# Kernel optimization log

Measured on AMD Instinct MI355X. Metric: run time of the kernel, lower is better.

Reference implementation:

```python
import jax, jax.numpy as jnp
import numpy as np
from jax import lax

H = 512          # hidden_dim
U = H // 2       # GRU units per direction
L = 3            # num_layers
B = 64           # num sequences
T = 512          # timesteps per sequence
EXTRA = 1000     # pass-through tail rows in `states`
RATE = 0.1       # dropout_rate
WSCALE = 0.05


def setup_inputs() -> dict:
    key = jax.random.key(0)
    ks = jax.random.split(key, 9)
    N = B * T + EXTRA
    states = jax.random.normal(ks[0], (N, H), jnp.float32)
    # prefix-valid mask: each sequence has a random valid length in [1, T]
    lengths = jax.random.randint(ks[1], (B,), 1, T + 1)
    mask2d = jnp.arange(T)[None, :] < lengths[:, None]          # [B, T]
    mask = jnp.concatenate([mask2d.reshape(-1), jnp.zeros((EXTRA,), bool)])
    # per-layer, per-direction GRU params (Keras reset_after=True layout):
    # kernel [H, 3U] (z|r|h), recurrent [U, 3U], bias [2, 3U] (input bias, recurrent bias)
    Wf = jax.random.normal(ks[2], (L, H, 3 * U), jnp.float32) * WSCALE
    Uf = jax.random.normal(ks[3], (L, U, 3 * U), jnp.float32) * WSCALE
    bf = jnp.zeros((L, 2, 3 * U), jnp.float32)
    Wb = jax.random.normal(ks[4], (L, H, 3 * U), jnp.float32) * WSCALE
    Ub = jax.random.normal(ks[5], (L, U, 3 * U), jnp.float32) * WSCALE
    bb = jnp.zeros((L, 2, 3 * U), jnp.float32)
    return {
        "states": states, "mask": mask, "seq_shape": (B, T), "training": 1,
        "Wf": Wf, "Uf": Uf, "bf": bf, "Wb": Wb, "Ub": Ub, "bb": bb,
    }


def _gru_scan(x, m, W, Uw, b):
    """Keras GRU (reset_after=True) over time with Keras mask semantics.
    x: [T, B, H], m: [T, B] bool. Returns outputs [T, B, U].
    Masked steps carry state (output = previous output)."""
    bi, br = b[0], b[1]
    xp = jnp.einsum('tbh,hk->tbk', x, W) + bi   # [T, B, 3U], hoisted input proj
    h0 = jnp.zeros((x.shape[1], U), x.dtype)

    def step(h, inp):
        xp_t, m_t = inp
        hp = h @ Uw + br                         # [B, 3U]
        xz, xr, xh = jnp.split(xp_t, 3, axis=-1)
        hz, hr, hh = jnp.split(hp, 3, axis=-1)
        z = jax.nn.sigmoid(xz + hz)
        r = jax.nn.sigmoid(xr + hr)
        hcand = jnp.tanh(xh + r * hh)
        hn = z * h + (1.0 - z) * hcand
        hn = jnp.where(m_t[:, None], hn, h)      # carry state through masked steps
        return hn, hn

    _, ys = lax.scan(step, h0, (xp, m))
    return ys


def _forward(states, mask, seq_shape, training, Wf, Uf, bf, Wb, Ub, bb):
    Bn, Tn = int(seq_shape[0]), int(seq_shape[1])
    total = Bn * Tn
    x = states[:total].reshape(Bn, Tn, H).transpose(1, 0, 2)  # [T, B, H]
    m = mask[:total].reshape(Bn, Tn).T                        # [T, B]
    rate = RATE * float(bool(training))
    dkey = jax.random.key(1234)
    for l in range(L):
        yf = _gru_scan(x, m, Wf[l], Uf[l], bf[l])
        yb = jnp.flip(_gru_scan(jnp.flip(x, 0), jnp.flip(m, 0), Wb[l], Ub[l], bb[l]), 0)
        x = jnp.concatenate([yf, yb], axis=-1)                # [T, B, H]
        if rate > 0.0:
            dkey, sk = jax.random.split(dkey)
            keep = jax.random.bernoulli(sk, 1.0 - rate, x.shape)
            x = jnp.where(keep, x / (1.0 - rate), 0.0)
    out = x.transpose(1, 0, 2).reshape(-1, H)                 # [B*T, H]
    return jnp.concatenate([out, states[total:]], axis=0)


def reference(states, mask, seq_shape, training, Wf, Uf, bf, Wb, Ub, bb):
    return _forward(states, mask, seq_shape, training, Wf, Uf, bf, Wb, Ub, bb)
```

## Files before the change

kernel.cpp:

```cpp
#include <hip/hip_runtime.h>
#include <stdint.h>

typedef __attribute__((ext_vector_type(8))) short short8;
typedef __attribute__((ext_vector_type(4))) float f32x4;

#define XB16_OFF  0UL
#define XP_OFF    33554432UL
#define WT_OFF    134217728UL
#define UT_OFF    138936320UL
#define BIASC_OFF 141295616UL
#define BRC_OFF   141314048UL
#define MASKT_OFF 141332480UL
#define FLAG_OFF  141725760UL

#define HB_STRIDE 264
#define HBLK (16 * HB_STRIDE)
#define LDS_BYTES (((size_t)256 * HB_STRIDE + 2 * HBLK) * 2)

#define LDS_BARRIER() asm volatile("s_waitcnt lgkmcnt(0)\n\ts_barrier" ::: "memory")

__host__ __device__ static inline void tf2x32(unsigned k0, unsigned k1,
                                              unsigned x0, unsigned x1,
                                              unsigned* o0, unsigned* o1) {
  unsigned ks2 = k0 ^ k1 ^ 0x1BD11BDAu;
#define TFR(r) { x0 += x1; x1 = (x1 << (r)) | (x1 >> (32 - (r))); x1 ^= x0; }
  x0 += k0; x1 += k1;
  TFR(13) TFR(15) TFR(26) TFR(6)   x0 += k1;  x1 += ks2 + 1u;
  TFR(17) TFR(29) TFR(16) TFR(24)  x0 += ks2; x1 += k0 + 2u;
  TFR(13) TFR(15) TFR(26) TFR(6)   x0 += k0;  x1 += k1 + 3u;
  TFR(17) TFR(29) TFR(16) TFR(24)  x0 += k1;  x1 += ks2 + 4u;
  TFR(13) TFR(15) TFR(26) TFR(6)   x0 += ks2; x1 += k0 + 5u;
#undef TFR
  *o0 = x0; *o1 = x1;
}

__device__ static inline short f2bf(float f) {
  unsigned u = __float_as_uint(f);
  u = (u + 0x7fffu + ((u >> 16) & 1u)) >> 16;
  return (short)u;
}
__device__ static inline float bf2f(short s) {
  unsigned u = ((unsigned)(unsigned short)s) << 16;
  return __uint_as_float(u);
}
__device__ static inline float cvt_lo(unsigned d) {
  union { unsigned short u; _Float16 h; } c; c.u = (unsigned short)(d & 0xffffu);
  return (float)c.h;
}
__device__ static inline float cvt_hi(unsigned d) {
  union { unsigned short u; _Float16 h; } c; c.u = (unsigned short)(d >> 16);
  return (float)c.h;
}

__global__ void init_k(unsigned* flag) {
  if (threadIdx.x == 0) *flag = 0u;
}

__global__ __launch_bounds__(256) void prep_k(
    const float* __restrict__ states, const unsigned* __restrict__ maskw,
    const float* __restrict__ Wf, const float* __restrict__ Uf,
    const float* __restrict__ bf_, const float* __restrict__ Wb,
    const float* __restrict__ Ub, const float* __restrict__ bb_,
    short* __restrict__ xb16, float* __restrict__ dout,
    short* __restrict__ Wt, short* __restrict__ Ut,
    float* __restrict__ biasc, float* __restrict__ brc,
    unsigned* __restrict__ flag) {
  const unsigned gid = blockIdx.x * 256 + threadIdx.x;
  {
    unsigned c = gid & 511u, rw = gid >> 9;
    unsigned t = rw >> 6, b = rw & 63u;
    xb16[gid] = f2bf(states[(size_t)(b * 512 + t) * 512 + c]);
  }
  if (gid < 512000u) dout[16777216u + gid] = states[16777216u + gid];
  if (gid < 2359296u) {
    unsigned l = gid / 786432u, rem = gid % 786432u;
    unsigned n = rem >> 9, k = rem & 511u;
    float s = (n < 768u) ? Wf[(size_t)(l * 512 + k) * 768 + n]
                         : Wb[(size_t)(l * 512 + k) * 768 + (n - 768u)];
    Wt[gid] = f2bf(s);
  }
  if (gid < 1179648u) {
    unsigned g = gid / 196608u, rem = gid % 196608u;
    unsigned dirv = g / 3u, l = g % 3u;
    unsigned n = rem >> 8, k = rem & 255u;
    const float* Usrc = dirv ? Ub : Uf;
    Ut[gid] = f2bf(Usrc[(size_t)(l * 256 + k) * 768 + n]);
  }
  if (gid < 4608u) {
    unsigned l = gid / 1536u, n = gid % 1536u;
    unsigned dirv = n / 768u, rem = n % 768u;
    const float* bsrc = dirv ? bb_ : bf_;
    float v = bsrc[(l * 2 + 0) * 768 + rem];
    if (rem < 512u) v += bsrc[(l * 2 + 1) * 768 + rem];
    biasc[gid] = v;
  }
  if (gid < 4608u) {
    unsigned g = gid / 768u, n = gid % 768u;
    unsigned dirv = g / 3u, l = g % 3u;
    brc[gid] = (dirv ? bb_ : bf_)[(l * 2 + 1) * 768 + n];
  }
  if (gid < 8192u) {
    if (maskw[gid] > 1u) atomicOr(flag, 1u);
  }
}

__global__ __launch_bounds__(256) void maskt_k(
    const unsigned char* __restrict__ mask8, const unsigned* __restrict__ flagp,
    unsigned char* __restrict__ maskt) {
  const unsigned gid = blockIdx.x * 256 + threadIdx.x;
  const unsigned b = gid >> 9, t = gid & 511u;
  const bool mbyte = (*flagp) != 0u;
  unsigned v = mbyte ? (unsigned)mask8[gid] : ((const unsigned*)mask8)[gid];
  maskt[t * 64 + b] = v ? 1u : 0u;
}

__global__ __launch_bounds__(256) void proj_gemm(
    const short* __restrict__ A, const short* __restrict__ Bt,
    const float* __restrict__ bias, _Float16* __restrict__ C) {
  __shared__ __align__(16) short As[4096];
  __shared__ __align__(16) short Bs[4096];
  const int tid = threadIdx.x;
  const int wave = tid >> 6, lane = tid & 63;
  const int col = lane & 15, kq = lane >> 4;
  const int wr = wave >> 1, wc = wave & 1;
  const int m0 = blockIdx.x * 128, n0 = blockIdx.y * 128;
  const uint4* Aq = (const uint4*)A;
  const uint4* Bq = (const uint4*)Bt;
  uint4* AsQ = (uint4*)As;
  uint4* BsQ = (uint4*)Bs;
  f32x4 acc[4][4];
#pragma unroll
  for (int i = 0; i < 4; ++i)
#pragma unroll
    for (int j = 0; j < 4; ++j) acc[i][j] = (f32x4){0.f, 0.f, 0.f, 0.f};

  for (int kt = 0; kt < 16; ++kt) {
    const int k8 = kt * 4;
#pragma unroll
    for (int rnd = 0; rnd < 2; ++rnd) {
      int chunk = rnd * 256 + tid;
      int row = chunk >> 2, kc = chunk & 3;
      AsQ[chunk] = Aq[(size_t)(m0 + row) * 64 + k8 + kc];
      BsQ[chunk] = Bq[(size_t)(n0 + row) * 64 + k8 + kc];
    }
    __syncthreads();
    short8 af[4], bfv[4];
#pragma unroll
    for (int i = 0; i < 4; ++i)
      af[i] = *(const short8*)(As + (wr * 64 + i * 16 + col) * 32 + kq * 8);
#pragma unroll
    for (int j = 0; j < 4; ++j)
      bfv[j] = *(const short8*)(Bs + (wc * 64 + j * 16 + col) * 32 + kq * 8);
#pragma unroll
    for (int i = 0; i < 4; ++i)
#pragma unroll
      for (int j = 0; j < 4; ++j)
        acc[i][j] = __builtin_amdgcn_mfma_f32_16x16x32_bf16(af[i], bfv[j], acc[i][j], 0, 0, 0);
    __syncthreads();
  }
#pragma unroll
  for (int j = 0; j < 4; ++j) {
    const int cg = n0 + wc * 64 + j * 16 + col;
    const float bv = bias[cg];
    const int dirv = cg / 768, rem = cg % 768;
    const int gate = rem >> 8, u = rem & 255;
    const size_t cbase =
        ((size_t)(((m0 >> 6) + wr) * 2 + dirv)) * 49152 + gate * 256 + u;
#pragma unroll
    for (int i = 0; i < 4; ++i) {
#pragma unroll
      for (int r = 0; r < 4; ++r)
        C[cbase + (size_t)(i * 16 + kq * 4 + r) * 768] = (_Float16)(acc[i][j][r] + bv);
    }
  }
}

__global__ __launch_bounds__(1024, 4) void gru16(
    const _Float16* __restrict__ xp, const short* __restrict__ UtAll,
    const float* __restrict__ brcAll, const unsigned char* __restrict__ maskt,
    short* __restrict__ yout, int layer) {
  extern __shared__ short lds[];
  short* hgate = lds;
  short* hbuf  = lds + 256 * HB_STRIDE;

  const int bid = blockIdx.x;
  const int dir = bid >> 2;
  const int b0 = (bid & 3) * 16;
  const int tid = threadIdx.x;
  const int wave = tid >> 6, lane = tid & 63;
  const int col = lane & 15, quad = lane >> 4;
  const int u0 = wave * 16 + quad * 4;
  const short* Ut = UtAll + (size_t)(dir * 3 + layer) * 768 * 256;
  const float* brc = brcAll + (dir * 3 + layer) * 768;

  const short* Uth = Ut + 512 * 256;
  for (int c = tid; c < 8192; c += 1024) {
    int row = c >> 5, q = c & 31;
    *(uint4*)(hgate + row * HB_STRIDE + q * 8) = *(const uint4*)(Uth + row * 256 + q * 8);
  }
  for (int i = tid; i < 2 * HBLK; i += 1024) hbuf[i] = 0;

  short8 zA[8], rA[8];
#pragma unroll
  for (int ks = 0; ks < 8; ++ks) {
    zA[ks] = *(const short8*)(Ut + (size_t)(wave * 16 + col) * 256 + ks * 32 + quad * 8);
    rA[ks] = *(const short8*)(Ut + (size_t)(256 + wave * 16 + col) * 256 + ks * 32 + quad * 8);
  }
  f32x4 brh;
#pragma unroll
  for (int r = 0; r < 4; ++r) brh[r] = brc[512 + u0 + r];

  const int t0 = dir ? 511 : 0;
  const int tstep = dir ? -1 : 1;
  const char* xpb = (const char*)xp;
  const int gb = b0 + col;
  unsigned xaddr = (unsigned)(((t0 * 2 + dir) * 64 + gb) * 1536 + wave * 32 + quad * 8);
  const int xstep = tstep * 196608;

  const short* hgA = hgate + (wave * 16 + col) * HB_STRIDE + quad * 8;
  const int rd_lane = col * HB_STRIDE + quad * 8;
  const int wr_lane = col * HB_STRIDE + u0;

  unsigned yoff = (unsigned)((t0 * 64 + gb) * 1024 + dir * 512 + u0 * 2);
  const int ystep = tstep * 65536;
  int moff = t0 * 64 + gb;

  uint2 pz, pr, ph;
  unsigned pm;
  pz = *(const uint2*)(xpb + xaddr);
  pr = *(const uint2*)(xpb + xaddr + 512);
  ph = *(const uint2*)(xpb + xaddr + 1024);
  pm = maskt[moff];

  float hp[4] = {0.f, 0.f, 0.f, 0.f};
  __syncthreads();

  for (int s = 0; s < 512; ++s) {
    f32x4 az, ar, ah;
    az[0] = cvt_lo(pz.x); az[1] = cvt_hi(pz.x);
    az[2] = cvt_lo(pz.y); az[3] = cvt_hi(pz.y);
    ar[0] = cvt_lo(pr.x); ar[1] = cvt_hi(pr.x);
    ar[2] = cvt_lo(pr.y); ar[3] = cvt_hi(pr.y);
    ah = brh;
    float xh[4];
    xh[0] = cvt_lo(ph.x); xh[1] = cvt_hi(ph.x);
    xh[2] = cvt_lo(ph.y); xh[3] = cvt_hi(ph.y);
    const bool mv = (pm != 0u);
    if (s < 511) {
      xaddr += xstep;
      pz = *(const uint2*)(xpb + xaddr);
      pr = *(const uint2*)(xpb + xaddr + 512);
      ph = *(const uint2*)(xpb + xaddr + 1024);
      moff += tstep * 64;
      pm = maskt[moff];
    }

    const short* hrd = hbuf + (s & 1) * HBLK + rd_lane;
#pragma unroll
    for (int ks = 0; ks < 8; ++ks) {
      short8 hbv = *(const short8*)(hrd + ks * 32);
      short8 hg  = *(const short8*)(hgA + ks * 32);
      az = __builtin_amdgcn_mfma_f32_16x16x32_bf16(zA[ks], hbv, az, 0, 0, 0);
      ar = __builtin_amdgcn_mfma_f32_16x16x32_bf16(rA[ks], hbv, ar, 0, 0, 0);
      ah = __builtin_amdgcn_mfma_f32_16x16x32_bf16(hg,     hbv, ah, 0, 0, 0);
    }

    float hn[4];
#pragma unroll
    for (int r = 0; r < 4; ++r) {
      float z  = 1.f / (1.f + __builtin_amdgcn_exp2f(az[r] * -1.44269504f));
      float rr = 1.f / (1.f + __builtin_amdgcn_exp2f(ar[r] * -1.44269504f));
      float pre = xh[r] + rr * ah[r];
      float hc = 1.f - 2.f / (__builtin_amdgcn_exp2f(pre * 2.88539008f) + 1.f);
      float hpv = hp[r];
      float v = hc + z * (hpv - hc);
      hn[r] = mv ? v : hpv;
      hp[r] = hn[r];
    }
    uint2 packed;
    asm("v_cvt_pk_bf16_f32 %0, %1, %2" : "=v"(packed.x) : "v"(hn[0]), "v"(hn[1]));
    asm("v_cvt_pk_bf16_f32 %0, %1, %2" : "=v"(packed.y) : "v"(hn[2]), "v"(hn[3]));
    *(uint2*)(hbuf + ((s & 1) ^ 1) * HBLK + wr_lane) = packed;
    *(uint2*)((char*)yout + yoff) = packed;
    yoff += ystep;
    LDS_BARRIER();
  }
}

__global__ __launch_bounds__(256) void drop_k(
    short* __restrict__ xb16, float* __restrict__ dout,
    const int* __restrict__ training, unsigned k0, unsigned k1, int last) {
  const unsigned gid = blockIdx.x * 256 + threadIdx.x;
  float v = bf2f(xb16[gid]);
  unsigned y0, y1;
  tf2x32(k0, k1, 0u, gid, &y0, &y1);
  unsigned bits = y0 ^ y1;
  float u = __uint_as_float((bits >> 9) | 0x3f800000u) - 1.0f;
  bool keep = u < 0.9f;
  int tr = *training;
  float ov = tr ? (keep ? v * (1.0f / 0.9f) : 0.0f) : v;
  if (last) {
    unsigned r = gid >> 9, c = gid & 511u;
    unsigned t = r >> 6, b = r & 63u;
    dout[(size_t)(b * 512 + t) * 512 + c] = ov;
  } else {
    xb16[gid] = f2bf(ov);
  }
}

extern "C" void kernel_launch(void* const* d_in, const int* in_sizes, int n_in,
                              void* d_out, int out_size, void* d_ws, size_t ws_size,
                              hipStream_t stream) {
  (void)in_sizes; (void)n_in; (void)out_size; (void)ws_size;
  const float* states = (const float*)d_in[0];
  const void*  mask   = d_in[1];
  const int*   training = (const int*)d_in[3];
  const float* Wf = (const float*)d_in[4];
  const float* Uf = (const float*)d_in[5];
  const float* bf_ = (const float*)d_in[6];
  const float* Wb = (const float*)d_in[7];
  const float* Ub = (const float*)d_in[8];
  const float* bb_ = (const float*)d_in[9];
  char* ws = (char*)d_ws;

  short* xb16   = (short*)(ws + XB16_OFF);
  _Float16* xp  = (_Float16*)(ws + XP_OFF);
  short* Wt     = (short*)(ws + WT_OFF);
  short* Ut     = (short*)(ws + UT_OFF);
  float* biasc  = (float*)(ws + BIASC_OFF);
  float* brc    = (float*)(ws + BRC_OFF);
  unsigned char* maskt = (unsigned char*)(ws + MASKT_OFF);
  unsigned* flag = (unsigned*)(ws + FLAG_OFF);
  float* dout = (float*)d_out;

  hipFuncSetAttribute((const void*)gru16,
                      hipFuncAttributeMaxDynamicSharedMemorySize, (int)LDS_BYTES);

  unsigned d0 = 0u, d1 = 1234u, sk0[3], sk1[3];
  for (int l = 0; l < 3; ++l) {
    unsigned a, b, c, d;
    tf2x32(d0, d1, 0u, 0u, &a, &b);
    tf2x32(d0, d1, 0u, 1u, &c, &d);
    sk0[l] = c; sk1[l] = d;
    d0 = a; d1 = b;
  }

  init_k<<<1, 64, 0, stream>>>(flag);
  prep_k<<<65536, 256, 0, stream>>>(states, (const unsigned*)mask, Wf, Uf, bf_,
                                    Wb, Ub, bb_, xb16, dout, Wt, Ut, biasc, brc, flag);
  maskt_k<<<128, 256, 0, stream>>>((const unsigned char*)mask, flag, maskt);
  for (int l = 0; l < 3; ++l) {
    proj_gemm<<<dim3(256, 12), 256, 0, stream>>>(xb16, Wt + (size_t)l * 1536 * 512,
                                                 biasc + l * 1536, xp);
    gru16<<<8, 1024, LDS_BYTES, stream>>>(xp, Ut, brc, maskt, xb16, l);
    drop_k<<<65536, 256, 0, stream>>>(xb16, dout, training, sk0[l], sk1[l], l == 2);
  }
}
```

Measured before the change: 3.797 ms.

## Halve GRU recurrence block to 8 waves, each computing 32 units

```diff
diff --git a/kernel.cpp b/kernel.cpp
--- a/kernel.cpp
+++ b/kernel.cpp
@@ -15,7 +15,7 @@
 
 #define HB_STRIDE 264
 #define HBLK (16 * HB_STRIDE)
-#define LDS_BYTES (((size_t)256 * HB_STRIDE + 2 * HBLK) * 2)
+#define LDS_BYTES (((size_t)128 * HB_STRIDE + 2 * HBLK) * 2)
 
 #define LDS_BARRIER() asm volatile("s_waitcnt lgkmcnt(0)\n\ts_barrier" ::: "memory")
 
@@ -175,13 +175,13 @@
   }
 }
 
-__global__ __launch_bounds__(1024, 4) void gru16(
+__global__ __launch_bounds__(512, 2) void gru32(
     const _Float16* __restrict__ xp, const short* __restrict__ UtAll,
     const float* __restrict__ brcAll, const unsigned char* __restrict__ maskt,
     short* __restrict__ yout, int layer) {
   extern __shared__ short lds[];
   short* hgate = lds;
-  short* hbuf  = lds + 256 * HB_STRIDE;
+  short* hbuf  = lds + 128 * HB_STRIDE;
 
   const int bid = blockIdx.x;
   const int dir = bid >> 2;
@@ -189,35 +189,44 @@
   const int tid = threadIdx.x;
   const int wave = tid >> 6, lane = tid & 63;
   const int col = lane & 15, quad = lane >> 4;
-  const int u0 = wave * 16 + quad * 4;
   const short* Ut = UtAll + (size_t)(dir * 3 + layer) * 768 * 256;
   const float* brc = brcAll + (dir * 3 + layer) * 768;
 
   const short* Uth = Ut + 512 * 256;
-  for (int c = tid; c < 8192; c += 1024) {
+  for (int c = tid; c < 4096; c += 512) {
     int row = c >> 5, q = c & 31;
-    *(uint4*)(hgate + row * HB_STRIDE + q * 8) = *(const uint4*)(Uth + row * 256 + q * 8);
-  }
-  for (int i = tid; i < 2 * HBLK; i += 1024) hbuf[i] = 0;
-
-  short8 zA[8], rA[8];
+    int u = ((row >> 4) << 5) + 16 + (row & 15);
+    *(uint4*)(hgate + row * HB_STRIDE + q * 8) = *(const uint4*)(Uth + u * 256 + q * 8);
+  }
+  for (int i = tid; i < 2 * HBLK; i += 512) hbuf[i] = 0;
+
+  short8 zA1[8], zA2[8], rA1[8], rA2[8], hA1[8];
+  const int m1 = wave * 32 + col;
 #pragma unroll
   for (int ks = 0; ks < 8; ++ks) {
-    zA[ks] = *(const short8*)(Ut + (size_t)(wave * 16 + col) * 256 + ks * 32 + quad * 8);
-    rA[ks] = *(const short8*)(Ut + (size_t)(256 + wave * 16 + col) * 256 + ks * 32 + quad * 8);
-  }
-  f32x4 brh;
-#pragma unroll
-  for (int r = 0; r < 4; ++r) brh[r] = brc[512 + u0 + r];
+    const int ko = ks * 32 + quad * 8;
+    zA1[ks] = *(const short8*)(Ut + (size_t)m1 * 256 + ko);
+    zA2[ks] = *(const short8*)(Ut + (size_t)(m1 + 16) * 256 + ko);
+    rA1[ks] = *(const short8*)(Ut + (size_t)(256 + m1) * 256 + ko);
+    rA2[ks] = *(const short8*)(Ut + (size_t)(256 + m1 + 16) * 256 + ko);
+    hA1[ks] = *(const short8*)(Ut + (size_t)(512 + m1) * 256 + ko);
+  }
+  const int u0 = wave * 32 + quad * 4;
+  f32x4 brh1, brh2;
+#pragma unroll
+  for (int r = 0; r < 4; ++r) {
+    brh1[r] = brc[512 + u0 + r];
+    brh2[r] = brc[512 + u0 + 16 + r];
+  }
 
   const int t0 = dir ? 511 : 0;
   const int tstep = dir ? -1 : 1;
   const char* xpb = (const char*)xp;
   const int gb = b0 + col;
-  unsigned xaddr = (unsigned)(((t0 * 2 + dir) * 64 + gb) * 1536 + wave * 32 + quad * 8);
+  unsigned xaddr = (unsigned)(((t0 * 2 + dir) * 64 + gb) * 1536 + wave * 64 + quad * 8);
   const int xstep = tstep * 196608;
 
-  const short* hgA = hgate + (wave * 16 + col) * HB_STRIDE + quad * 8;
+  const short* hg2 = hgate + (wave * 16 + col) * HB_STRIDE + quad * 8;
   const int rd_lane = col * HB_STRIDE + quad * 8;
   const int wr_lane = col * HB_STRIDE + u0;
 
@@ -225,32 +234,44 @@
   const int ystep = tstep * 65536;
   int moff = t0 * 64 + gb;
 
-  uint2 pz, pr, ph;
+  uint2 pz1, pz2, pr1, pr2, ph1, ph2;
   unsigned pm;
-  pz = *(const uint2*)(xpb + xaddr);
-  pr = *(const uint2*)(xpb + xaddr + 512);
-  ph = *(const uint2*)(xpb + xaddr + 1024);
+  pz1 = *(const uint2*)(xpb + xaddr);
+  pz2 = *(const uint2*)(xpb + xaddr + 32);
+  pr1 = *(const uint2*)(xpb + xaddr + 512);
+  pr2 = *(const uint2*)(xpb + xaddr + 544);
+  ph1 = *(const uint2*)(xpb + xaddr + 1024);
+  ph2 = *(const uint2*)(xpb + xaddr + 1056);
   pm = maskt[moff];
 
-  float hp[4] = {0.f, 0.f, 0.f, 0.f};
+  float hp[8] = {0.f, 0.f, 0.f, 0.f, 0.f, 0.f, 0.f, 0.f};
   __syncthreads();
 
   for (int s = 0; s < 512; ++s) {
-    f32x4 az, ar, ah;
-    az[0] = cvt_lo(pz.x); az[1] = cvt_hi(pz.x);
-    az[2] = cvt_lo(pz.y); az[3] = cvt_hi(pz.y);
-    ar[0] = cvt_lo(pr.x); ar[1] = cvt_hi(pr.x);
-    ar[2] = cvt_lo(pr.y); ar[3] = cvt_hi(pr.y);
-    ah = brh;
-    float xh[4];
-    xh[0] = cvt_lo(ph.x); xh[1] = cvt_hi(ph.x);
-    xh[2] = cvt_lo(ph.y); xh[3] = cvt_hi(ph.y);
+    f32x4 az1, az2, ar1, ar2, ah1, ah2;
+    az1[0] = cvt_lo(pz1.x); az1[1] = cvt_hi(pz1.x);
+    az1[2] = cvt_lo(pz1.y); az1[3] = cvt_hi(pz1.y);
+    az2[0] = cvt_lo(pz2.x); az2[1] = cvt_hi(pz2.x);
+    az2[2] = cvt_lo(pz2.y); az2[3] = cvt_hi(pz2.y);
+    ar1[0] = cvt_lo(pr1.x); ar1[1] = cvt_hi(pr1.x);
+    ar1[2] = cvt_lo(pr1.y); ar1[3] = cvt_hi(pr1.y);
+    ar2[0] = cvt_lo(pr2.x); ar2[1] = cvt_hi(pr2.x);
+    ar2[2] = cvt_lo(pr2.y); ar2[3] = cvt_hi(pr2.y);
+    ah1 = brh1; ah2 = brh2;
+    float xh[8];
+    xh[0] = cvt_lo(ph1.x); xh[1] = cvt_hi(ph1.x);
+    xh[2] = cvt_lo(ph1.y); xh[3] = cvt_hi(ph1.y);
+    xh[4] = cvt_lo(ph2.x); xh[5] = cvt_hi(ph2.x);
+    xh[6] = cvt_lo(ph2.y); xh[7] = cvt_hi(ph2.y);
     const bool mv = (pm != 0u);
     if (s < 511) {
       xaddr += xstep;
-      pz = *(const uint2*)(xpb + xaddr);
-      pr = *(const uint2*)(xpb + xaddr + 512);
-      ph = *(const uint2*)(xpb + xaddr + 1024);
+      pz1 = *(const uint2*)(xpb + xaddr);
+      pz2 = *(const uint2*)(xpb + xaddr + 32);
+      pr1 = *(const uint2*)(xpb + xaddr + 512);
+      pr2 = *(const uint2*)(xpb + xaddr + 544);
+      ph1 = *(const uint2*)(xpb + xaddr + 1024);
+      ph2 = *(const uint2*)(xpb + xaddr + 1056);
       moff += tstep * 64;
       pm = maskt[moff];
     }
@@ -259,29 +280,49 @@
 #pragma unroll
     for (int ks = 0; ks < 8; ++ks) {
       short8 hbv = *(const short8*)(hrd + ks * 32);
-      short8 hg  = *(const short8*)(hgA + ks * 32);
-      az = __builtin_amdgcn_mfma_f32_16x16x32_bf16(zA[ks], hbv, az, 0, 0, 0);
-      ar = __builtin_amdgcn_mfma_f32_16x16x32_bf16(rA[ks], hbv, ar, 0, 0, 0);
-      ah = __builtin_amdgcn_mfma_f32_16x16x32_bf16(hg,     hbv, ah, 0, 0, 0);
-    }
-
-    float hn[4];
+      short8 h2  = *(const short8*)(hg2 + ks * 32);
+      az1 = __builtin_amdgcn_mfma_f32_16x16x32_bf16(zA1[ks], hbv, az1, 0, 0, 0);
+      az2 = __builtin_amdgcn_mfma_f32_16x16x32_bf16(zA2[ks], hbv, az2, 0, 0, 0);
+      ar1 = __builtin_amdgcn_mfma_f32_16x16x32_bf16(rA1[ks], hbv, ar1, 0, 0, 0);
+      ar2 = __builtin_amdgcn_mfma_f32_16x16x32_bf16(rA2[ks], hbv, ar2, 0, 0, 0);
+      ah1 = __builtin_amdgcn_mfma_f32_16x16x32_bf16(hA1[ks], hbv, ah1, 0, 0, 0);
+      ah2 = __builtin_amdgcn_mfma_f32_16x16x32_bf16(h2,      hbv, ah2, 0, 0, 0);
+    }
+
+    float hn[8];
 #pragma unroll
     for (int r = 0; r < 4; ++r) {
-      float z  = 1.f / (1.f + __builtin_amdgcn_exp2f(az[r] * -1.44269504f));
-      float rr = 1.f / (1.f + __builtin_amdgcn_exp2f(ar[r] * -1.44269504f));
-      float pre = xh[r] + rr * ah[r];
+      float z  = 1.f / (1.f + __builtin_amdgcn_exp2f(az1[r] * -1.44269504f));
+      float rr = 1.f / (1.f + __builtin_amdgcn_exp2f(ar1[r] * -1.44269504f));
+      float pre = xh[r] + rr * ah1[r];
       float hc = 1.f - 2.f / (__builtin_amdgcn_exp2f(pre * 2.88539008f) + 1.f);
       float hpv = hp[r];
       float v = hc + z * (hpv - hc);
       hn[r] = mv ? v : hpv;
       hp[r] = hn[r];
     }
-    uint2 packed;
-    asm("v_cvt_pk_bf16_f32 %0, %1, %2" : "=v"(packed.x) : "v"(hn[0]), "v"(hn[1]));
-    asm("v_cvt_pk_bf16_f32 %0, %1, %2" : "=v"(packed.y) : "v"(hn[2]), "v"(hn[3]));
-    *(uint2*)(hbuf + ((s & 1) ^ 1) * HBLK + wr_lane) = packed;
-    *(uint2*)((char*)yout + yoff) = packed;
+#pragma unroll
+    for (int r = 0; r < 4; ++r) {
+      float z  = 1.f / (1.f + __builtin_amdgcn_exp2f(az2[r] * -1.44269504f));
+      float rr = 1.f / (1.f + __builtin_amdgcn_exp2f(ar2[r] * -1.44269504f));
+      float pre = xh[4 + r] + rr * ah2[r];
+      float hc = 1.f - 2.f / (__builtin_amdgcn_exp2f(pre * 2.88539008f) + 1.f);
+      float hpv = hp[4 + r];
+      float v = hc + z * (hpv - hc);
+      hn[4 + r] = mv ? v : hpv;
+      hp[4 + r] = hn[4 + r];
+    }
+    uint2 pk1, pk2;
+    asm("v_cvt_pk_bf16_f32 %0, %1, %2" : "=v"(pk1.x) : "v"(hn[0]), "v"(hn[1]));
+    asm("v_cvt_pk_bf16_f32 %0, %1, %2" : "=v"(pk1.y) : "v"(hn[2]), "v"(hn[3]));
+    asm("v_cvt_pk_bf16_f32 %0, %1, %2" : "=v"(pk2.x) : "v"(hn[4]), "v"(hn[5]));
+    asm("v_cvt_pk_bf16_f32 %0, %1, %2" : "=v"(pk2.y) : "v"(hn[6]), "v"(hn[7]));
+    short* hwr = hbuf + ((s & 1) ^ 1) * HBLK + wr_lane;
+    *(uint2*)(hwr) = pk1;
+    *(uint2*)(hwr + 16) = pk2;
+    char* yb = (char*)yout + yoff;
+    *(uint2*)(yb) = pk1;
+    *(uint2*)(yb + 32) = pk2;
     yoff += ystep;
     LDS_BARRIER();
   }
@@ -333,7 +374,7 @@
   unsigned* flag = (unsigned*)(ws + FLAG_OFF);
   float* dout = (float*)d_out;
 
-  hipFuncSetAttribute((const void*)gru16,
+  hipFuncSetAttribute((const void*)gru32,
                       hipFuncAttributeMaxDynamicSharedMemorySize, (int)LDS_BYTES);
 
   unsigned d0 = 0u, d1 = 1234u, sk0[3], sk1[3];
@@ -352,7 +393,7 @@
   for (int l = 0; l < 3; ++l) {
     proj_gemm<<<dim3(256, 12), 256, 0, stream>>>(xb16, Wt + (size_t)l * 1536 * 512,
                                                  biasc + l * 1536, xp);
-    gru16<<<8, 1024, LDS_BYTES, stream>>>(xp, Ut, brc, maskt, xb16, l);
+    gru32<<<8, 512, LDS_BYTES, stream>>>(xp, Ut, brc, maskt, xb16, l);
     drop_k<<<65536, 256, 0, stream>>>(xb16, dout, training, sk0[l], sk1[l], l == 2);
   }
 }
```

Measured after the change: 4.830 ms. 27.2% more time.

## Keep half of recurrent h-gate weights in registers, use direct global-to-LDS loads

Applied to the files above, without the earlier changes.

```diff
diff --git a/kernel.cpp b/kernel.cpp
--- a/kernel.cpp
+++ b/kernel.cpp
@@ -15,9 +15,15 @@
 
 #define HB_STRIDE 264
 #define HBLK (16 * HB_STRIDE)
-#define LDS_BYTES (((size_t)256 * HB_STRIDE + 2 * HBLK) * 2)
+#define HG_STRIDE 136
+#define LDS_BYTES (((size_t)256 * HG_STRIDE + 2 * HBLK) * 2)
 
 #define LDS_BARRIER() asm volatile("s_waitcnt lgkmcnt(0)\n\ts_barrier" ::: "memory")
+
+typedef __attribute__((address_space(1))) const unsigned int* as1_u32p;
+typedef __attribute__((address_space(3))) unsigned int* as3_u32p;
+#define GLOBAL_TO_LDS16(g, l) \
+  __builtin_amdgcn_global_load_lds((as1_u32p)(g), (as3_u32p)(l), 16, 0, 0)
 
 __host__ __device__ static inline void tf2x32(unsigned k0, unsigned k1,
                                               unsigned x0, unsigned x1,
@@ -126,8 +132,6 @@
   const int m0 = blockIdx.x * 128, n0 = blockIdx.y * 128;
   const uint4* Aq = (const uint4*)A;
   const uint4* Bq = (const uint4*)Bt;
-  uint4* AsQ = (uint4*)As;
-  uint4* BsQ = (uint4*)Bs;
   f32x4 acc[4][4];
 #pragma unroll
   for (int i = 0; i < 4; ++i)
@@ -138,10 +142,11 @@
     const int k8 = kt * 4;
 #pragma unroll
     for (int rnd = 0; rnd < 2; ++rnd) {
-      int chunk = rnd * 256 + tid;
-      int row = chunk >> 2, kc = chunk & 3;
-      AsQ[chunk] = Aq[(size_t)(m0 + row) * 64 + k8 + kc];
-      BsQ[chunk] = Bq[(size_t)(n0 + row) * 64 + k8 + kc];
+      const int chunk = rnd * 256 + wave * 64 + lane;
+      const int row = chunk >> 2, kc = chunk & 3;
+      const int base = (rnd * 256 + wave * 64) * 8;
+      GLOBAL_TO_LDS16(&Aq[(size_t)(m0 + row) * 64 + k8 + kc], As + base);
+      GLOBAL_TO_LDS16(&Bq[(size_t)(n0 + row) * 64 + k8 + kc], Bs + base);
     }
     __syncthreads();
     short8 af[4], bfv[4];
@@ -181,7 +186,7 @@
     short* __restrict__ yout, int layer) {
   extern __shared__ short lds[];
   short* hgate = lds;
-  short* hbuf  = lds + 256 * HB_STRIDE;
+  short* hbuf  = lds + 256 * HG_STRIDE;
 
   const int bid = blockIdx.x;
   const int dir = bid >> 2;
@@ -194,18 +199,22 @@
   const float* brc = brcAll + (dir * 3 + layer) * 768;
 
   const short* Uth = Ut + 512 * 256;
-  for (int c = tid; c < 8192; c += 1024) {
-    int row = c >> 5, q = c & 31;
-    *(uint4*)(hgate + row * HB_STRIDE + q * 8) = *(const uint4*)(Uth + row * 256 + q * 8);
+  for (int c = tid; c < 4096; c += 1024) {
+    int row = c >> 4, q = c & 15;
+    *(uint4*)(hgate + row * HG_STRIDE + q * 8) =
+        *(const uint4*)(Uth + row * 256 + 128 + q * 8);
   }
   for (int i = tid; i < 2 * HBLK; i += 1024) hbuf[i] = 0;
 
-  short8 zA[8], rA[8];
+  short8 zA[8], rA[8], hA[4];
 #pragma unroll
   for (int ks = 0; ks < 8; ++ks) {
     zA[ks] = *(const short8*)(Ut + (size_t)(wave * 16 + col) * 256 + ks * 32 + quad * 8);
     rA[ks] = *(const short8*)(Ut + (size_t)(256 + wave * 16 + col) * 256 + ks * 32 + quad * 8);
   }
+#pragma unroll
+  for (int ks = 0; ks < 4; ++ks)
+    hA[ks] = *(const short8*)(Ut + (size_t)(512 + wave * 16 + col) * 256 + ks * 32 + quad * 8);
   f32x4 brh;
 #pragma unroll
   for (int r = 0; r < 4; ++r) brh[r] = brc[512 + u0 + r];
@@ -217,7 +226,7 @@
   unsigned xaddr = (unsigned)(((t0 * 2 + dir) * 64 + gb) * 1536 + wave * 32 + quad * 8);
   const int xstep = tstep * 196608;
 
-  const short* hgA = hgate + (wave * 16 + col) * HB_STRIDE + quad * 8;
+  const short* hgL = hgate + (wave * 16 + col) * HG_STRIDE + quad * 8;
   const int rd_lane = col * HB_STRIDE + quad * 8;
   const int wr_lane = col * HB_STRIDE + u0;
 
@@ -225,51 +234,42 @@
   const int ystep = tstep * 65536;
   int moff = t0 * 64 + gb;
 
-  uint2 pz, pr, ph;
-  unsigned pm;
-  pz = *(const uint2*)(xpb + xaddr);
-  pr = *(const uint2*)(xpb + xaddr + 512);
-  ph = *(const uint2*)(xpb + xaddr + 1024);
-  pm = maskt[moff];
-
   float hp[4] = {0.f, 0.f, 0.f, 0.f};
   __syncthreads();
 
   for (int s = 0; s < 512; ++s) {
-    f32x4 az, ar, ah;
-    az[0] = cvt_lo(pz.x); az[1] = cvt_hi(pz.x);
-    az[2] = cvt_lo(pz.y); az[3] = cvt_hi(pz.y);
-    ar[0] = cvt_lo(pr.x); ar[1] = cvt_hi(pr.x);
-    ar[2] = cvt_lo(pr.y); ar[3] = cvt_hi(pr.y);
-    ah = brh;
-    float xh[4];
-    xh[0] = cvt_lo(ph.x); xh[1] = cvt_hi(ph.x);
-    xh[2] = cvt_lo(ph.y); xh[3] = cvt_hi(ph.y);
-    const bool mv = (pm != 0u);
-    if (s < 511) {
-      xaddr += xstep;
-      pz = *(const uint2*)(xpb + xaddr);
-      pr = *(const uint2*)(xpb + xaddr + 512);
-      ph = *(const uint2*)(xpb + xaddr + 1024);
-      moff += tstep * 64;
-      pm = maskt[moff];
-    }
+    uint2 pz = *(const uint2*)(xpb + xaddr);
+    uint2 pr = *(const uint2*)(xpb + xaddr + 512);
+    uint2 ph = *(const uint2*)(xpb + xaddr + 1024);
+    unsigned pm = maskt[moff];
+
+    f32x4 az = {0.f, 0.f, 0.f, 0.f};
+    f32x4 ar = {0.f, 0.f, 0.f, 0.f};
+    f32x4 ah = brh;
 
     const short* hrd = hbuf + (s & 1) * HBLK + rd_lane;
 #pragma unroll
     for (int ks = 0; ks < 8; ++ks) {
       short8 hbv = *(const short8*)(hrd + ks * 32);
-      short8 hg  = *(const short8*)(hgA + ks * 32);
+      short8 hg  = (ks < 4) ? hA[ks] : *(const short8*)(hgL + (ks - 4) * 32);
       az = __builtin_amdgcn_mfma_f32_16x16x32_bf16(zA[ks], hbv, az, 0, 0, 0);
       ar = __builtin_amdgcn_mfma_f32_16x16x32_bf16(rA[ks], hbv, ar, 0, 0, 0);
       ah = __builtin_amdgcn_mfma_f32_16x16x32_bf16(hg,     hbv, ah, 0, 0, 0);
     }
 
+    const bool mv = (pm != 0u);
+    float xz[4], xr[4], xh[4];
+    xz[0] = cvt_lo(pz.x); xz[1] = cvt_hi(pz.x);
+    xz[2] = cvt_lo(pz.y); xz[3] = cvt_hi(pz.y);
+    xr[0] = cvt_lo(pr.x); xr[1] = cvt_hi(pr.x);
+    xr[2] = cvt_lo(pr.y); xr[3] = cvt_hi(pr.y);
+    xh[0] = cvt_lo(ph.x); xh[1] = cvt_hi(ph.x);
+    xh[2] = cvt_lo(ph.y); xh[3] = cvt_hi(ph.y);
     float hn[4];
 #pragma unroll
     for (int r = 0; r < 4; ++r) {
-      float z  = 1.f / (1.f + __builtin_amdgcn_exp2f(az[r] * -1.44269504f));
-      float rr = 1.f / (1.f + __builtin_amdgcn_exp2f(ar[r] * -1.44269504f));
+      float z  = 1.f / (1.f + __builtin_amdgcn_exp2f((az[r] + xz[r]) * -1.44269504f));
+      float rr = 1.f / (1.f + __builtin_amdgcn_exp2f((ar[r] + xr[r]) * -1.44269504f));
       float pre = xh[r] + rr * ah[r];
       float hc = 1.f - 2.f / (__builtin_amdgcn_exp2f(pre * 2.88539008f) + 1.f);
       float hpv = hp[r];
@@ -283,6 +283,8 @@
     *(uint2*)(hbuf + ((s & 1) ^ 1) * HBLK + wr_lane) = packed;
     *(uint2*)((char*)yout + yoff) = packed;
     yoff += ystep;
+    xaddr += xstep;
+    moff += tstep * 64;
     LDS_BARRIER();
   }
 }
```

New measurement: 4.556 ms. 20.0% more time.
